# Optimization experiments

Hardware: AMD Instinct MI355X
Metric: run time of the kernel (lower is better)

Reference implementation:

```python
import jax, jax.numpy as jnp
import numpy as np

N_NODES = 200000
N_EDGES = 800000
C1, E1 = 20000, 80000
C2, E2 = 2000, 8000
N_IN, N_HID, K_BLOCK = 24, 64, 6
N_OUT = 6
BN_EPS = 1e-5


def cheb_conv(x, edge_index, W, b, n):
    """PyG ChebConv with lambda_max=2: L_hat = -D^-1/2 A D^-1/2."""
    src, dst = edge_index[0], edge_index[1]
    K = W.shape[0]
    deg = jax.ops.segment_sum(jnp.ones(src.shape[0], x.dtype), dst, num_segments=n)
    dis = jnp.where(deg > 0, 1.0 / jnp.sqrt(jnp.maximum(deg, 1.0)), 0.0)
    norm = -(dis[src] * dis[dst])[:, None]  # [E,1]

    def prop(h):
        return jax.ops.segment_sum(h[src] * norm, dst, num_segments=n)

    Tx0 = x
    out = Tx0 @ W[0]
    if K > 1:
        Tx1 = prop(Tx0)
        out = out + Tx1 @ W[1]
        for k in range(2, K):
            Tx2 = 2.0 * prop(Tx1) - Tx0
            out = out + Tx2 @ W[k]
            Tx0, Tx1 = Tx1, Tx2
    return out + b


def batchnorm(h, g, bt):
    m = jnp.mean(h, axis=0)
    v = jnp.mean((h - m) ** 2, axis=0)  # biased var, as torch BN forward
    return (h - m) / jnp.sqrt(v + BN_EPS) * g + bt


def kipf_block(x, edge_index, W, b, g, bt, n):
    return jax.nn.relu(batchnorm(cheb_conv(x, edge_index, W, b, n), g, bt))


def segment_mean(x, seg, n_seg):
    s = jax.ops.segment_sum(x, seg, num_segments=n_seg)
    cnt = jax.ops.segment_sum(jnp.ones(x.shape[0], x.dtype), seg, num_segments=n_seg)
    return s / jnp.maximum(cnt, 1.0)[:, None]


def setup_inputs() -> dict:
    key = jax.random.key(0)
    ks = jax.random.split(key, 12)
    inp = {
        "x": jax.random.normal(ks[0], (N_NODES, N_IN), jnp.float32),
        "edge_index": jax.random.randint(ks[1], (2, N_EDGES), 0, N_NODES),
        "cluster1": jax.random.randint(ks[2], (N_NODES,), 0, C1),
        "cluster2": jax.random.randint(ks[3], (N_NODES,), 0, C2),
        "edge_index_c1": jax.random.randint(ks[4], (2, E1), 0, C1),
        "edge_index_c2": jax.random.randint(ks[5], (2, E2), 0, C2),
    }
    sc = 1.0 / np.sqrt(N_IN * K_BLOCK)
    for i, kk in zip((1, 2, 3), (ks[6], ks[7], ks[8])):
        inp[f"W{i}"] = jax.random.normal(kk, (K_BLOCK, N_IN, N_HID), jnp.float32) * sc
        inp[f"b{i}"] = jnp.zeros((N_HID,), jnp.float32)
        inp[f"g{i}"] = jnp.ones((N_HID,), jnp.float32)
        inp[f"bt{i}"] = jnp.zeros((N_HID,), jnp.float32)
    n_mix = 3 * N_HID + N_IN
    inp["Wm"] = jax.random.normal(ks[9], (1, n_mix, N_OUT), jnp.float32) / np.sqrt(n_mix)
    inp["bm"] = jnp.zeros((N_OUT,), jnp.float32)
    return inp


def reference(x, edge_index, cluster1, cluster2, edge_index_c1, edge_index_c2,
              W1, b1, g1, bt1, W2, b2, g2, bt2, W3, b3, g3, bt3, Wm, bm):
    # branch 1: full-resolution graph
    h1 = kipf_block(x, edge_index, W1, b1, g1, bt1, N_NODES)
    # branch 2: cluster1-pooled graph, then unpool
    xp1 = segment_mean(x, cluster1, C1)
    h2 = kipf_block(xp1, edge_index_c1, W2, b2, g2, bt2, C1)[cluster1]
    # branch 3: cluster2-pooled graph, then unpool
    xp2 = segment_mean(x, cluster2, C2)
    h3 = kipf_block(xp2, edge_index_c2, W3, b3, g3, bt3, C2)[cluster2]
    # skip concat with raw input, then mixing conv (K=1 -> identity Cheb term)
    mix = jnp.concatenate([h1, h2, h3, x], axis=1)
    return cheb_conv(mix, edge_index, Wm, bm, N_NODES)
```

## Files before the change

kernel.cpp:

```cpp
#include <hip/hip_runtime.h>
#include <algorithm>

#define FIN 24
#define NHID 64
#define NMIX 216
#define NOUT 6
#define BN_EPS 1e-5f

__global__ void k_hist(const int* __restrict__ ei, int E, int* deg) {
    int e = blockIdx.x * blockDim.x + threadIdx.x;
    if (e < E) atomicAdd(&deg[ei[E + e]], 1);
}

__global__ void k_scan_local(const int* __restrict__ deg, int n, int* rowptr, int* bsum,
                             float* __restrict__ dis) {
    __shared__ int s[256];
    int i = blockIdx.x * 256 + threadIdx.x;
    int v = (i < n) ? deg[i] : 0;
    if (i < n) dis[i] = v > 0 ? rsqrtf((float)v) : 0.f;
    s[threadIdx.x] = v;
    __syncthreads();
#pragma unroll
    for (int off = 1; off < 256; off <<= 1) {
        int x = (threadIdx.x >= off) ? s[threadIdx.x - off] : 0;
        __syncthreads();
        s[threadIdx.x] += x;
        __syncthreads();
    }
    if (i <= n) rowptr[i] = s[threadIdx.x] - v;
    if (threadIdx.x == 255) bsum[blockIdx.x] = s[255];
}

__global__ void k_scan_bsum(int* bsum, int nb) {
    __shared__ int s[256];
    int carry = 0;
    for (int base = 0; base < nb; base += 256) {
        int i = base + threadIdx.x;
        int v = (i < nb) ? bsum[i] : 0;
        s[threadIdx.x] = v;
        __syncthreads();
#pragma unroll
        for (int off = 1; off < 256; off <<= 1) {
            int x = (threadIdx.x >= off) ? s[threadIdx.x - off] : 0;
            __syncthreads();
            s[threadIdx.x] += x;
            __syncthreads();
        }
        if (i < nb) bsum[i] = s[threadIdx.x] - v + carry;
        carry += s[255];
        __syncthreads();
    }
}

__global__ void k_scan_add(int* rowptr, const int* __restrict__ bsum, int n) {
    int i = blockIdx.x * 256 + threadIdx.x;
    if (i <= n) rowptr[i] += bsum[blockIdx.x];
}

__global__ void k_fill(const int* __restrict__ ei, int E, const float* __restrict__ dis,
                       const int* __restrict__ rowptr, int* fill, int2* __restrict__ cv) {
    int e = blockIdx.x * blockDim.x + threadIdx.x;
    if (e >= E) return;
    int s = ei[e], d = ei[E + e];
    int slot = rowptr[d] + atomicAdd(&fill[d], 1);
    cv[slot] = make_int2(s, __float_as_int(-dis[s] * dis[d]));
}

__global__ void k_wt3(const float* __restrict__ Wa, float* __restrict__ Ta,
                      const float* __restrict__ Wb, float* __restrict__ Tb,
                      const float* __restrict__ Wc, float* __restrict__ Tc) {
    int o = blockIdx.x * blockDim.x + threadIdx.x;
    int which = o / 9216, oo = o - which * 9216;
    const float* W = (which == 0) ? Wa : (which == 1) ? Wb : Wc;
    float* T       = (which == 0) ? Ta : (which == 1) ? Tb : Tc;
    int k = oo / 1536, r = oo - k * 1536;
    int j = r / FIN, f = r - j * FIN;
    T[oo] = W[k * 1536 + f * NHID + j];
}

__global__ void k_propg(const int* __restrict__ rowptr, const int2* __restrict__ cv,
                        float scale, const float* __restrict__ h,
                        const float* __restrict__ prev, float* __restrict__ out, int n) {
    int idx = blockIdx.x * blockDim.x + threadIdx.x;
    if (idx >= n * 6) return;
    int d = idx / 6, q = idx - d * 6;
    int beg = rowptr[d], end = rowptr[d + 1];
    const float4* h4 = reinterpret_cast<const float4*>(h);
    float ax = 0.f, ay = 0.f, az = 0.f, aw = 0.f;
    float bx = 0.f, by = 0.f, bz = 0.f, bw = 0.f;
    int e = beg;
    for (; e + 2 <= end; e += 2) {
        int2 c0 = cv[e], c1 = cv[e + 1];
        float w0 = __int_as_float(c0.y), w1 = __int_as_float(c1.y);
        float4 h0 = h4[(size_t)c0.x * 6 + q];
        float4 h1 = h4[(size_t)c1.x * 6 + q];
        ax = fmaf(w0, h0.x, ax); ay = fmaf(w0, h0.y, ay);
        az = fmaf(w0, h0.z, az); aw = fmaf(w0, h0.w, aw);
        bx = fmaf(w1, h1.x, bx); by = fmaf(w1, h1.y, by);
        bz = fmaf(w1, h1.z, bz); bw = fmaf(w1, h1.w, bw);
    }
    if (e < end) {
        int2 c0 = cv[e];
        float w0 = __int_as_float(c0.y);
        float4 h0 = h4[(size_t)c0.x * 6 + q];
        ax = fmaf(w0, h0.x, ax); ay = fmaf(w0, h0.y, ay);
        az = fmaf(w0, h0.z, az); aw = fmaf(w0, h0.w, aw);
    }
    ax += bx; ay += by; az += bz; aw += bw;
    float4 r;
    if (prev) {
        float4 pv = reinterpret_cast<const float4*>(prev)[idx];
        r = make_float4(fmaf(scale, ax, -pv.x), fmaf(scale, ay, -pv.y),
                        fmaf(scale, az, -pv.z), fmaf(scale, aw, -pv.w));
    } else {
        r = make_float4(scale * ax, scale * ay, scale * az, scale * aw);
    }
    reinterpret_cast<float4*>(out)[idx] = r;
}

__global__ void k_gemv2(const float* __restrict__ S1, const float* __restrict__ S2,
                        const float* __restrict__ Wta, const float* __restrict__ Wtb,
                        const float* __restrict__ bias, float* __restrict__ acc,
                        float* __restrict__ stats, int n) {
    __shared__ float sb[4][2][16 * FIN];
    int j = threadIdx.x & 63;
    int w = threadIdx.x >> 6;
    int nbase = blockIdx.x * 64 + w * 16;
    float4 wa4[6], wb4[6];
    {
        const float4* pa = reinterpret_cast<const float4*>(Wta + j * FIN);
        const float4* pb = reinterpret_cast<const float4*>(Wtb + j * FIN);
#pragma unroll
        for (int t = 0; t < 6; ++t) { wa4[t] = pa[t]; wb4[t] = pb[t]; }
    }
#pragma unroll
    for (int k = 0; k < 3; ++k) {
        int i = k * 64 + j;
        int half = i / 96;
        int j4 = i - half * 96;
        int nd = j4 / 6, q = j4 - nd * 6;
        int node = nbase + nd;
        const float* src = (half ? S2 : S1) + (size_t)node * FIN + q * 4;
        float4 v = (node < n) ? *reinterpret_cast<const float4*>(src)
                              : make_float4(0.f, 0.f, 0.f, 0.f);
        *reinterpret_cast<float4*>(&sb[w][half][j4 * 4]) = v;
    }
    float sum = 0.f, sq = 0.f;
#pragma unroll 2
    for (int nd = 0; nd < 16; ++nd) {
        int node = nbase + nd;
        bool ok = (node < n);
        float base = bias ? bias[j] : (ok ? acc[(size_t)node * NHID + j] : 0.f);
        const float4* r1 = reinterpret_cast<const float4*>(&sb[w][0][nd * FIN]);
        const float4* r2 = reinterpret_cast<const float4*>(&sb[w][1][nd * FIN]);
        float a = 0.f, p = 0.f;
#pragma unroll
        for (int t = 0; t < 6; ++t) {
            float4 v = r1[t];
            a = fmaf(v.x, wa4[t].x, a);
            p = fmaf(v.y, wa4[t].y, p);
            a = fmaf(v.z, wa4[t].z, a);
            p = fmaf(v.w, wa4[t].w, p);
        }
#pragma unroll
        for (int t = 0; t < 6; ++t) {
            float4 v = r2[t];
            a = fmaf(v.x, wb4[t].x, a);
            p = fmaf(v.y, wb4[t].y, p);
            a = fmaf(v.z, wb4[t].z, a);
            p = fmaf(v.w, wb4[t].w, p);
        }
        float r = base + a + p;
        if (ok) {
            acc[(size_t)node * NHID + j] = r;
            sum += r; sq = fmaf(r, r, sq);
        }
    }
    if (stats) {
        __shared__ float rs[256], rq[256];
        rs[threadIdx.x] = sum; rq[threadIdx.x] = sq;
        __syncthreads();
        if (threadIdx.x < 64) {
            float s = rs[threadIdx.x] + rs[threadIdx.x + 64] + rs[threadIdx.x + 128] + rs[threadIdx.x + 192];
            float q = rq[threadIdx.x] + rq[threadIdx.x + 64] + rq[threadIdx.x + 128] + rq[threadIdx.x + 192];
            atomicAdd(&stats[threadIdx.x], s);
            atomicAdd(&stats[NHID + threadIdx.x], q);
        }
    }
}

__global__ void k_bnprep3(const float* __restrict__ st1, const float* __restrict__ g1,
                          const float* __restrict__ bt1, float inv1,
                          const float* __restrict__ st2, const float* __restrict__ g2,
                          const float* __restrict__ bt2, float inv2,
                          const float* __restrict__ st3, const float* __restrict__ g3,
                          const float* __restrict__ bt3, float inv3,
                          float* __restrict__ s1, float* __restrict__ s2,
                          float* __restrict__ s3) {
    int b = threadIdx.x >> 6, i = threadIdx.x & 63;
    const float* st = (b == 0) ? st1 : (b == 1) ? st2 : st3;
    const float* g  = (b == 0) ? g1  : (b == 1) ? g2  : g3;
    const float* bt = (b == 0) ? bt1 : (b == 1) ? bt2 : bt3;
    float inv       = (b == 0) ? inv1 : (b == 1) ? inv2 : inv3;
    float* so       = (b == 0) ? s1  : (b == 1) ? s2  : s3;
    float m = st[i] * inv;
    float v = st[NHID + i] * inv - m * m;
    float sc = g[i] * rsqrtf(v + BN_EPS);
    so[i] = sc;
    so[NHID + i] = fmaf(-m, sc, bt[i]);
}

__global__ void k_scatter(const float* __restrict__ x, const int* __restrict__ cl,
                          int n, float* xp, float* cnt) {
    int idx = blockIdx.x * blockDim.x + threadIdx.x;
    if (idx >= n * FIN) return;
    int node = idx / FIN, f = idx - node * FIN;
    int c = cl[node];
    atomicAdd(&xp[c * FIN + f], x[idx]);
    if (f == 0) atomicAdd(&cnt[c], 1.f);
}

__global__ void k_divcnt(float* xp, const float* __restrict__ cnt, int c) {
    int idx = blockIdx.x * blockDim.x + threadIdx.x;
    if (idx >= c * FIN) return;
    xp[idx] = xp[idx] / fmaxf(cnt[idx / FIN], 1.f);
}

__global__ void k_final(const float* __restrict__ acc1, const float* __restrict__ sc1,
                        const float* __restrict__ h2, const float* __restrict__ sc2,
                        const int* __restrict__ cl1,
                        const float* __restrict__ h3, const float* __restrict__ sc3,
                        const int* __restrict__ cl2,
                        const float* __restrict__ x, const float* __restrict__ Wm,
                        const float* __restrict__ bm, float* __restrict__ out, int n) {
    int t = blockIdx.x * blockDim.x + threadIdx.x;
    if (t >= n) return;
    float o[NOUT];
#pragma unroll
    for (int j = 0; j < NOUT; ++j) o[j] = bm[j];
    {
        const float4* r4 = reinterpret_cast<const float4*>(acc1 + (size_t)t * NHID);
#pragma unroll
        for (int i4 = 0; i4 < NHID / 4; ++i4) {
            float4 v = r4[i4];
            float hv[4] = {v.x, v.y, v.z, v.w};
#pragma unroll
            for (int c = 0; c < 4; ++c) {
                int i = i4 * 4 + c;
                float h = fmaxf(fmaf(hv[c], sc1[i], sc1[NHID + i]), 0.f);
#pragma unroll
                for (int j = 0; j < NOUT; ++j) o[j] = fmaf(h, Wm[i * NOUT + j], o[j]);
            }
        }
    }
    {
        const float4* r4 = reinterpret_cast<const float4*>(h2 + (size_t)cl1[t] * NHID);
#pragma unroll
        for (int i4 = 0; i4 < NHID / 4; ++i4) {
            float4 v = r4[i4];
            float hv[4] = {v.x, v.y, v.z, v.w};
#pragma unroll
            for (int c = 0; c < 4; ++c) {
                int hid = i4 * 4 + c;
                float h = fmaxf(fmaf(hv[c], sc2[hid], sc2[NHID + hid]), 0.f);
#pragma unroll
                for (int j = 0; j < NOUT; ++j) o[j] = fmaf(h, Wm[(NHID + hid) * NOUT + j], o[j]);
            }
        }
    }
    {
        const float4* r4 = reinterpret_cast<const float4*>(h3 + (size_t)cl2[t] * NHID);
#pragma unroll
        for (int i4 = 0; i4 < NHID / 4; ++i4) {
            float4 v = r4[i4];
            float hv[4] = {v.x, v.y, v.z, v.w};
#pragma unroll
            for (int c = 0; c < 4; ++c) {
                int hid = i4 * 4 + c;
                float h = fmaxf(fmaf(hv[c], sc3[hid], sc3[NHID + hid]), 0.f);
#pragma unroll
                for (int j = 0; j < NOUT; ++j) o[j] = fmaf(h, Wm[(2 * NHID + hid) * NOUT + j], o[j]);
            }
        }
    }
    {
        const float4* r4 = reinterpret_cast<const float4*>(x + (size_t)t * FIN);
#pragma unroll
        for (int i4 = 0; i4 < FIN / 4; ++i4) {
            float4 v = r4[i4];
            float hv[4] = {v.x, v.y, v.z, v.w};
#pragma unroll
            for (int c = 0; c < 4; ++c) {
                int i = 3 * NHID + i4 * 4 + c;
#pragma unroll
                for (int j = 0; j < NOUT; ++j) o[j] = fmaf(hv[c], Wm[i * NOUT + j], o[j]);
            }
        }
    }
    float* op = out + (size_t)t * NOUT;
#pragma unroll
    for (int j = 0; j < NOUT; ++j) op[j] = o[j];
}

extern "C" void kernel_launch(void* const* d_in, const int* in_sizes, int n_in,
                              void* d_out, int out_size, void* d_ws, size_t ws_size,
                              hipStream_t stream) {
    const int N = 200000, E = 800000;
    const int C1n = 20000, E1 = 80000;
    const int C2n = 2000, E2 = 8000;

    const float* x  = (const float*)d_in[0];
    const int* ei   = (const int*)d_in[1];
    const int* cl1  = (const int*)d_in[2];
    const int* cl2  = (const int*)d_in[3];
    const int* eic1 = (const int*)d_in[4];
    const int* eic2 = (const int*)d_in[5];
    const float* W1 = (const float*)d_in[6];  const float* b1 = (const float*)d_in[7];
    const float* g1 = (const float*)d_in[8];  const float* bt1 = (const float*)d_in[9];
    const float* W2 = (const float*)d_in[10]; const float* b2 = (const float*)d_in[11];
    const float* g2 = (const float*)d_in[12]; const float* bt2 = (const float*)d_in[13];
    const float* W3 = (const float*)d_in[14]; const float* b3 = (const float*)d_in[15];
    const float* g3 = (const float*)d_in[16]; const float* bt3 = (const float*)d_in[17];
    const float* Wm = (const float*)d_in[18]; const float* bm = (const float*)d_in[19];

    char* wb = (char*)d_ws;
    size_t off = 0;
    auto alloc = [&](size_t nwords) {
        void* p = wb + off; off += ((nwords + 3) & ~(size_t)3) * 4; return p;
    };
    int* degi1 = (int*)alloc(N);   int* fill1 = (int*)alloc(N);
    int* degi2 = (int*)alloc(C1n); int* fill2 = (int*)alloc(C1n);
    int* degi3 = (int*)alloc(C2n); int* fill3 = (int*)alloc(C2n);
    float* st1 = (float*)alloc(128); float* st2 = (float*)alloc(128); float* st3 = (float*)alloc(128);
    float* xp1 = (float*)alloc((size_t)C1n * FIN); float* cnt1 = (float*)alloc(C1n);
    float* xp2 = (float*)alloc((size_t)C2n * FIN); float* cnt2 = (float*)alloc(C2n);
    size_t zero_bytes = off;
    int* rp1 = (int*)alloc(N + 1);   int2* cv1 = (int2*)alloc(2 * (size_t)E);
    int* rp2 = (int*)alloc(C1n + 1); int2* cv2 = (int2*)alloc(2 * (size_t)E1);
    int* rp3 = (int*)alloc(C2n + 1); int2* cv3 = (int2*)alloc(2 * (size_t)E2);
    float* dis1 = (float*)alloc(N); float* dis2 = (float*)alloc(C1n); float* dis3 = (float*)alloc(C2n);
    int* bsum = (int*)alloc(1024);
    float* scsh1 = (float*)alloc(128); float* scsh2 = (float*)alloc(128); float* scsh3 = (float*)alloc(128);
    float* Wt1 = (float*)alloc(9216); float* Wt2 = (float*)alloc(9216); float* Wt3 = (float*)alloc(9216);
    float* B1_0 = (float*)alloc((size_t)N * FIN);   float* B1_1 = (float*)alloc((size_t)N * FIN);
    float* B2_0 = (float*)alloc((size_t)C1n * FIN); float* B2_1 = (float*)alloc((size_t)C1n * FIN);
    float* B3_0 = (float*)alloc((size_t)C2n * FIN); float* B3_1 = (float*)alloc((size_t)C2n * FIN);
    float* acc1 = (float*)alloc((size_t)N * NHID);
    float* acc2 = (float*)alloc((size_t)C1n * NHID);
    float* acc3 = (float*)alloc((size_t)C2n * NHID);
    if (off > ws_size) return;

    hipMemsetAsync(d_ws, 0, zero_bytes, stream);

    const int T = 256;
    auto cdiv = [](int a, int b) { return (a + b - 1) / b; };

    k_wt3<<<cdiv(3 * 9216, T), T, 0, stream>>>(W1, Wt1, W2, Wt2, W3, Wt3);

    auto branch = [&](const float* xin, int n, const int* e, int Ecnt,
                      const float* Wt, const float* bb, int* degi, int* fill, float* dis,
                      int* rp, int2* cv, float* B0, float* Bb1, float* acc, float* st) {
        int ge = cdiv(Ecnt, T), gn = cdiv(n, T);
        int nb = cdiv(n + 1, 256);
        int gg = cdiv(n, 64);
        int gp = cdiv(n * 6, T);
        const int WSZ = NHID * FIN;
        k_hist<<<ge, T, 0, stream>>>(e, Ecnt, degi);
        k_scan_local<<<nb, 256, 0, stream>>>(degi, n, rp, bsum, dis);
        k_scan_bsum<<<1, 256, 0, stream>>>(bsum, nb);
        k_scan_add<<<nb, 256, 0, stream>>>(rp, bsum, n);
        k_fill<<<ge, T, 0, stream>>>(e, Ecnt, dis, rp, fill, cv);
        k_propg<<<gp, T, 0, stream>>>(rp, cv, 1.0f, xin, nullptr, B0, n);
        k_gemv2<<<gg, T, 0, stream>>>(xin, B0, Wt, Wt + WSZ, bb, acc, nullptr, n);
        k_propg<<<gp, T, 0, stream>>>(rp, cv, 2.0f, B0, xin, Bb1, n);
        k_propg<<<gp, T, 0, stream>>>(rp, cv, 2.0f, Bb1, B0, B0, n);
        k_gemv2<<<gg, T, 0, stream>>>(Bb1, B0, Wt + 2 * WSZ, Wt + 3 * WSZ, nullptr, acc, nullptr, n);
        k_propg<<<gp, T, 0, stream>>>(rp, cv, 2.0f, B0, Bb1, Bb1, n);
        k_propg<<<gp, T, 0, stream>>>(rp, cv, 2.0f, Bb1, B0, B0, n);
        k_gemv2<<<gg, T, 0, stream>>>(Bb1, B0, Wt + 4 * WSZ, Wt + 5 * WSZ, nullptr, acc, st, n);
    };

    branch(x, N, ei, E, Wt1, b1, degi1, fill1, dis1, rp1, cv1, B1_0, B1_1, acc1, st1);
    k_scatter<<<cdiv(N * FIN, T), T, 0, stream>>>(x, cl1, N, xp1, cnt1);
    k_divcnt<<<cdiv(C1n * FIN, T), T, 0, stream>>>(xp1, cnt1, C1n);
    branch(xp1, C1n, eic1, E1, Wt2, b2, degi2, fill2, dis2, rp2, cv2, B2_0, B2_1, acc2, st2);
    k_scatter<<<cdiv(N * FIN, T), T, 0, stream>>>(x, cl2, N, xp2, cnt2);
    k_divcnt<<<cdiv(C2n * FIN, T), T, 0, stream>>>(xp2, cnt2, C2n);
    branch(xp2, C2n, eic2, E2, Wt3, b3, degi3, fill3, dis3, rp3, cv3, B3_0, B3_1, acc3, st3);
    k_bnprep3<<<1, 192, 0, stream>>>(st1, g1, bt1, 1.0f / (float)N,
                                     st2, g2, bt2, 1.0f / (float)C1n,
                                     st3, g3, bt3, 1.0f / (float)C2n,
                                     scsh1, scsh2, scsh3);
    k_final<<<cdiv(N, T), T, 0, stream>>>(acc1, scsh1, acc2, scsh2, cl1,
                                          acc3, scsh3, cl2,
                                          x, Wm, bm, (float*)d_out, N);
}
```

Before: 680.8 us.

## Materialize all Chebyshev terms then apply one fused six-term GEMV

Keeps every Chebyshev term in its own buffer and replaces three two-term GEMV passes with a single kernel that accumulates all six terms in registers. This removes two read-modify-write passes over the 64-wide accumulator (N×64 floats each) and two launches per branch. In exchange it needs five term buffers instead of two, and the fused kernel uses more shared memory per block (six staged inputs), which may reduce occupancy.

```diff
diff --git a/kernel.cpp b/kernel.cpp
--- a/kernel.cpp
+++ b/kernel.cpp
@@ -118,74 +118,76 @@
     reinterpret_cast<float4*>(out)[idx] = r;
 }
 
-__global__ void k_gemv2(const float* __restrict__ S1, const float* __restrict__ S2,
-                        const float* __restrict__ Wta, const float* __restrict__ Wtb,
-                        const float* __restrict__ bias, float* __restrict__ acc,
-                        float* __restrict__ stats, int n) {
-    __shared__ float sb[4][2][16 * FIN];
+__global__ void k_gemv6(const float* __restrict__ S0, const float* __restrict__ S1,
+                        const float* __restrict__ S2, const float* __restrict__ S3,
+                        const float* __restrict__ S4, const float* __restrict__ S5,
+                        const float* __restrict__ Wt, const float* __restrict__ bias,
+                        float* __restrict__ acc, float* __restrict__ stats, int n) {
+    __shared__ float sb[4][6][16 * FIN];
     int j = threadIdx.x & 63;
     int w = threadIdx.x >> 6;
     int nbase = blockIdx.x * 64 + w * 16;
-    float4 wa4[6], wb4[6];
-    {
-        const float4* pa = reinterpret_cast<const float4*>(Wta + j * FIN);
-        const float4* pb = reinterpret_cast<const float4*>(Wtb + j * FIN);
-#pragma unroll
-        for (int t = 0; t < 6; ++t) { wa4[t] = pa[t]; wb4[t] = pb[t]; }
-    }
-#pragma unroll
-    for (int k = 0; k < 3; ++k) {
+#pragma unroll
+    for (int k = 0; k < 9; ++k) {
         int i = k * 64 + j;
         int half = i / 96;
         int j4 = i - half * 96;
         int nd = j4 / 6, q = j4 - nd * 6;
         int node = nbase + nd;
-        const float* src = (half ? S2 : S1) + (size_t)node * FIN + q * 4;
+        const float* Sh = (half == 0) ? S0 : (half == 1) ? S1 : (half == 2) ? S2
+                        : (half == 3) ? S3 : (half == 4) ? S4 : S5;
+        const float* src = Sh + (size_t)node * FIN + q * 4;
         float4 v = (node < n) ? *reinterpret_cast<const float4*>(src)
                               : make_float4(0.f, 0.f, 0.f, 0.f);
         *reinterpret_cast<float4*>(&sb[w][half][j4 * 4]) = v;
     }
+    float accv[16];
+    {
+        float bb = bias[j];
+#pragma unroll
+        for (int nd = 0; nd < 16; ++nd) accv[nd] = bb;
+    }
+#pragma unroll 1
+    for (int k = 0; k < 6; ++k) {
+        const float4* wp = reinterpret_cast<const float4*>(Wt + k * (NHID * FIN) + j * FIN);
+        float4 w0 = wp[0], w1 = wp[1], w2 = wp[2], w3 = wp[3], w4 = wp[4], w5 = wp[5];
+#pragma unroll
+        for (int nd = 0; nd < 16; ++nd) {
+            const float4* r = reinterpret_cast<const float4*>(&sb[w][k][nd * FIN]);
+            float4 v0 = r[0], v1 = r[1], v2 = r[2], v3 = r[3], v4 = r[4], v5 = r[5];
+            float a = accv[nd];
+            a = fmaf(v0.x, w0.x, a); a = fmaf(v0.y, w0.y, a);
+            a = fmaf(v0.z, w0.z, a); a = fmaf(v0.w, w0.w, a);
+            a = fmaf(v1.x, w1.x, a); a = fmaf(v1.y, w1.y, a);
+            a = fmaf(v1.z, w1.z, a); a = fmaf(v1.w, w1.w, a);
+            a = fmaf(v2.x, w2.x, a); a = fmaf(v2.y, w2.y, a);
+            a = fmaf(v2.z, w2.z, a); a = fmaf(v2.w, w2.w, a);
+            a = fmaf(v3.x, w3.x, a); a = fmaf(v3.y, w3.y, a);
+            a = fmaf(v3.z, w3.z, a); a = fmaf(v3.w, w3.w, a);
+            a = fmaf(v4.x, w4.x, a); a = fmaf(v4.y, w4.y, a);
+            a = fmaf(v4.z, w4.z, a); a = fmaf(v4.w, w4.w, a);
+            a = fmaf(v5.x, w5.x, a); a = fmaf(v5.y, w5.y, a);
+            a = fmaf(v5.z, w5.z, a); a = fmaf(v5.w, w5.w, a);
+            accv[nd] = a;
+        }
+    }
     float sum = 0.f, sq = 0.f;
-#pragma unroll 2
+#pragma unroll
     for (int nd = 0; nd < 16; ++nd) {
         int node = nbase + nd;
-        bool ok = (node < n);
-        float base = bias ? bias[j] : (ok ? acc[(size_t)node * NHID + j] : 0.f);
-        const float4* r1 = reinterpret_cast<const float4*>(&sb[w][0][nd * FIN]);
-        const float4* r2 = reinterpret_cast<const float4*>(&sb[w][1][nd * FIN]);
-        float a = 0.f, p = 0.f;
-#pragma unroll
-        for (int t = 0; t < 6; ++t) {
-            float4 v = r1[t];
-            a = fmaf(v.x, wa4[t].x, a);
-            p = fmaf(v.y, wa4[t].y, p);
-            a = fmaf(v.z, wa4[t].z, a);
-            p = fmaf(v.w, wa4[t].w, p);
-        }
-#pragma unroll
-        for (int t = 0; t < 6; ++t) {
-            float4 v = r2[t];
-            a = fmaf(v.x, wb4[t].x, a);
-            p = fmaf(v.y, wb4[t].y, p);
-            a = fmaf(v.z, wb4[t].z, a);
-            p = fmaf(v.w, wb4[t].w, p);
-        }
-        float r = base + a + p;
-        if (ok) {
-            acc[(size_t)node * NHID + j] = r;
-            sum += r; sq = fmaf(r, r, sq);
-        }
-    }
-    if (stats) {
-        __shared__ float rs[256], rq[256];
-        rs[threadIdx.x] = sum; rq[threadIdx.x] = sq;
-        __syncthreads();
-        if (threadIdx.x < 64) {
-            float s = rs[threadIdx.x] + rs[threadIdx.x + 64] + rs[threadIdx.x + 128] + rs[threadIdx.x + 192];
-            float q = rq[threadIdx.x] + rq[threadIdx.x + 64] + rq[threadIdx.x + 128] + rq[threadIdx.x + 192];
-            atomicAdd(&stats[threadIdx.x], s);
-            atomicAdd(&stats[NHID + threadIdx.x], q);
-        }
+        if (node < n) {
+            acc[(size_t)node * NHID + j] = accv[nd];
+            sum += accv[nd]; sq = fmaf(accv[nd], accv[nd], sq);
+        }
+    }
+    __shared__ float rs[256], rq[256];
+    rs[threadIdx.x] = sum; rq[threadIdx.x] = sq;
+    __syncthreads();
+    if (threadIdx.x < 64) {
+        float s = rs[threadIdx.x] + rs[threadIdx.x + 64] + rs[threadIdx.x + 128] + rs[threadIdx.x + 192];
+        float q = rq[threadIdx.x] + rq[threadIdx.x + 64] + rq[threadIdx.x + 128] + rq[threadIdx.x + 192];
+        atomicAdd(&stats[threadIdx.x], s);
+        atomicAdd(&stats[NHID + threadIdx.x], q);
     }
 }
 
@@ -342,9 +344,9 @@
     int* bsum = (int*)alloc(1024);
     float* scsh1 = (float*)alloc(128); float* scsh2 = (float*)alloc(128); float* scsh3 = (float*)alloc(128);
     float* Wt1 = (float*)alloc(9216); float* Wt2 = (float*)alloc(9216); float* Wt3 = (float*)alloc(9216);
-    float* B1_0 = (float*)alloc((size_t)N * FIN);   float* B1_1 = (float*)alloc((size_t)N * FIN);
-    float* B2_0 = (float*)alloc((size_t)C1n * FIN); float* B2_1 = (float*)alloc((size_t)C1n * FIN);
-    float* B3_0 = (float*)alloc((size_t)C2n * FIN); float* B3_1 = (float*)alloc((size_t)C2n * FIN);
+    float* T1[5]; for (int i = 0; i < 5; ++i) T1[i] = (float*)alloc((size_t)N * FIN);
+    float* T2[5]; for (int i = 0; i < 5; ++i) T2[i] = (float*)alloc((size_t)C1n * FIN);
+    float* T3[5]; for (int i = 0; i < 5; ++i) T3[i] = (float*)alloc((size_t)C2n * FIN);
     float* acc1 = (float*)alloc((size_t)N * NHID);
     float* acc2 = (float*)alloc((size_t)C1n * NHID);
     float* acc3 = (float*)alloc((size_t)C2n * NHID);
@@ -359,34 +361,32 @@
 
     auto branch = [&](const float* xin, int n, const int* e, int Ecnt,
                       const float* Wt, const float* bb, int* degi, int* fill, float* dis,
-                      int* rp, int2* cv, float* B0, float* Bb1, float* acc, float* st) {
-        int ge = cdiv(Ecnt, T), gn = cdiv(n, T);
+                      int* rp, int2* cv, float** Tb, float* acc, float* st) {
+        int ge = cdiv(Ecnt, T);
         int nb = cdiv(n + 1, 256);
         int gg = cdiv(n, 64);
         int gp = cdiv(n * 6, T);
-        const int WSZ = NHID * FIN;
         k_hist<<<ge, T, 0, stream>>>(e, Ecnt, degi);
         k_scan_local<<<nb, 256, 0, stream>>>(degi, n, rp, bsum, dis);
         k_scan_bsum<<<1, 256, 0, stream>>>(bsum, nb);
         k_scan_add<<<nb, 256, 0, stream>>>(rp, bsum, n);
         k_fill<<<ge, T, 0, stream>>>(e, Ecnt, dis, rp, fill, cv);
-        k_propg<<<gp, T, 0, stream>>>(rp, cv, 1.0f, xin, nullptr, B0, n);
-        k_gemv2<<<gg, T, 0, stream>>>(xin, B0, Wt, Wt + WSZ, bb, acc, nullptr, n);
-        k_propg<<<gp, T, 0, stream>>>(rp, cv, 2.0f, B0, xin, Bb1, n);
-        k_propg<<<gp, T, 0, stream>>>(rp, cv, 2.0f, Bb1, B0, B0, n);
-        k_gemv2<<<gg, T, 0, stream>>>(Bb1, B0, Wt + 2 * WSZ, Wt + 3 * WSZ, nullptr, acc, nullptr, n);
-        k_propg<<<gp, T, 0, stream>>>(rp, cv, 2.0f, B0, Bb1, Bb1, n);
-        k_propg<<<gp, T, 0, stream>>>(rp, cv, 2.0f, Bb1, B0, B0, n);
-        k_gemv2<<<gg, T, 0, stream>>>(Bb1, B0, Wt + 4 * WSZ, Wt + 5 * WSZ, nullptr, acc, st, n);
+        k_propg<<<gp, T, 0, stream>>>(rp, cv, 1.0f, xin, nullptr, Tb[0], n);
+        k_propg<<<gp, T, 0, stream>>>(rp, cv, 2.0f, Tb[0], xin, Tb[1], n);
+        k_propg<<<gp, T, 0, stream>>>(rp, cv, 2.0f, Tb[1], Tb[0], Tb[2], n);
+        k_propg<<<gp, T, 0, stream>>>(rp, cv, 2.0f, Tb[2], Tb[1], Tb[3], n);
+        k_propg<<<gp, T, 0, stream>>>(rp, cv, 2.0f, Tb[3], Tb[2], Tb[4], n);
+        k_gemv6<<<gg, T, 0, stream>>>(xin, Tb[0], Tb[1], Tb[2], Tb[3], Tb[4],
+                                      Wt, bb, acc, st, n);
     };
 
-    branch(x, N, ei, E, Wt1, b1, degi1, fill1, dis1, rp1, cv1, B1_0, B1_1, acc1, st1);
+    branch(x, N, ei, E, Wt1, b1, degi1, fill1, dis1, rp1, cv1, T1, acc1, st1);
     k_scatter<<<cdiv(N * FIN, T), T, 0, stream>>>(x, cl1, N, xp1, cnt1);
     k_divcnt<<<cdiv(C1n * FIN, T), T, 0, stream>>>(xp1, cnt1, C1n);
-    branch(xp1, C1n, eic1, E1, Wt2, b2, degi2, fill2, dis2, rp2, cv2, B2_0, B2_1, acc2, st2);
+    branch(xp1, C1n, eic1, E1, Wt2, b2, degi2, fill2, dis2, rp2, cv2, T2, acc2, st2);
     k_scatter<<<cdiv(N * FIN, T), T, 0, stream>>>(x, cl2, N, xp2, cnt2);
     k_divcnt<<<cdiv(C2n * FIN, T), T, 0, stream>>>(xp2, cnt2, C2n);
-    branch(xp2, C2n, eic2, E2, Wt3, b3, degi3, fill3, dis3, rp3, cv3, B3_0, B3_1, acc3, st3);
+    branch(xp2, C2n, eic2, E2, Wt3, b3, degi3, fill3, dis3, rp3, cv3, T3, acc3, st3);
     k_bnprep3<<<1, 192, 0, stream>>>(st1, g1, bt1, 1.0f / (float)N,
                                      st2, g2, bt2, 1.0f / (float)C1n,
                                      st3, g3, bt3, 1.0f / (float)C2n,
```

After: 658.9 us. 3.2% less time.
